# Kernel optimization log

Hardware: AMD Instinct MI355X
Metric: run time of the kernel (lower is better)

The kernel has to match this reference:

```python
import jax, jax.numpy as jnp
import numpy as np

N_AST = 200000
N_TEST = 10000
H = 128
NUM_AST_LABELS = 128
AST_CONTENT = 256
NUM_CLASSES = 2
N_LAYERS = 5
E_AA, E_AT, E_TA = 2000000, 500000, 500000


def seg_mean(msg, dst, n):
    # mean aggregation of edge messages per destination node
    s = jax.ops.segment_sum(msg, dst, num_segments=n)
    d = jax.ops.segment_sum(jnp.ones((dst.shape[0], 1), msg.dtype), dst, num_segments=n)
    return s / jnp.maximum(d, 1.0)


def gcn_layer(h_ast, h_test, src_aa, dst_aa, src_at, dst_at, src_ta, dst_ta,
              W_aa, W_at, W_ta, b_ast, b_test):
    # transform-then-aggregate per canonical edge type, sum over edge types per dst ntype
    m_aa = seg_mean((h_ast @ W_aa)[src_aa], dst_aa, N_AST)
    m_ta = seg_mean((h_test @ W_ta)[src_ta], dst_ta, N_AST)
    new_ast = jax.nn.relu(m_aa + m_ta + b_ast)
    m_at = seg_mean((h_ast @ W_at)[src_at], dst_at, N_TEST)
    new_test = jax.nn.relu(m_at + b_test)
    return new_ast, new_test


def setup_inputs() -> dict:
    key = jax.random.key(0)
    ks = jax.random.split(key, 16)
    Hh = H // 2
    inp = {
        "ast_label": jax.random.randint(ks[0], (N_AST,), 0, NUM_AST_LABELS),
        "ast_content": jax.random.normal(ks[1], (N_AST, AST_CONTENT), jnp.float32),
        "src_aa": jax.random.randint(ks[2], (E_AA,), 0, N_AST, jnp.int32),
        "dst_aa": jax.random.randint(ks[3], (E_AA,), 0, N_AST, jnp.int32),
        "src_at": jax.random.randint(ks[4], (E_AT,), 0, N_AST, jnp.int32),
        "dst_at": jax.random.randint(ks[5], (E_AT,), 0, N_TEST, jnp.int32),
        "src_ta": jax.random.randint(ks[6], (E_TA,), 0, N_TEST, jnp.int32),
        "dst_ta": jax.random.randint(ks[7], (E_TA,), 0, N_AST, jnp.int32),
        "n_test": N_TEST,
        "ast_label_emb": jax.random.normal(ks[8], (NUM_AST_LABELS, Hh), jnp.float32) * 0.1,
        "ast_content_W": jax.random.normal(ks[9], (AST_CONTENT, Hh), jnp.float32) * (1.0 / np.sqrt(AST_CONTENT)),
        "ast_content_b": jax.random.normal(ks[10], (Hh,), jnp.float32) * 0.1,
        "test_embedding": jax.random.normal(ks[11], (H,), jnp.float32),
        "W_aa": jax.random.normal(ks[12], (N_LAYERS, H, H), jnp.float32) * (1.0 / np.sqrt(H)),
        "W_at": jax.random.normal(ks[13], (N_LAYERS, H, H), jnp.float32) * (1.0 / np.sqrt(H)),
        "W_ta": jax.random.normal(ks[14], (N_LAYERS, H, H), jnp.float32) * (1.0 / np.sqrt(H)),
        "b_ast": jnp.zeros((N_LAYERS, H), jnp.float32),
        "b_test": jnp.zeros((N_LAYERS, H), jnp.float32),
        "dec_W": jax.random.normal(ks[15], (H, NUM_CLASSES), jnp.float32) * (1.0 / np.sqrt(H)),
        "dec_b": jnp.zeros((NUM_CLASSES,), jnp.float32),
    }
    return inp


def reference(ast_label, ast_content, src_aa, dst_aa, src_at, dst_at, src_ta, dst_ta,
              n_test, ast_label_emb, ast_content_W, ast_content_b, test_embedding,
              W_aa, W_at, W_ta, b_ast, b_test, dec_W, dec_b):
    # hetero node encoding: ast = [embedding(label) || linear(content)], test = broadcast learned vector
    h_ast = jnp.concatenate(
        [ast_label_emb[ast_label], ast_content @ ast_content_W + ast_content_b], axis=-1)
    h_test = jnp.broadcast_to(test_embedding[None, :], (n_test, H))

    def layer(i, ha, ht):
        return gcn_layer(ha, ht, src_aa, dst_aa, src_at, dst_at, src_ta, dst_ta,
                         W_aa[i], W_at[i], W_ta[i], b_ast[i], b_test[i])

    h_ast, h_test = layer(0, h_ast, h_test)
    res_a, res_t = h_ast, h_test
    h_ast, h_test = layer(1, h_ast, h_test)
    h_ast, h_test = res_a + h_ast, res_t + h_test
    h_ast, h_test = layer(2, h_ast, h_test)
    res_a, res_t = h_ast, h_test
    h_ast, h_test = layer(3, h_ast, h_test)
    h_ast, h_test = res_a + h_ast, res_t + h_test
    h_ast, h_test = layer(4, h_ast, h_test)

    logits = h_ast @ dec_W + dec_b  # ast_decode_node_func with num_classes>1 -> softmax
    pred = jax.nn.softmax(logits, axis=1)
    return logits, pred
```

## Files before the change

kernel.cpp:

```cpp
#include <hip/hip_runtime.h>

#define N_ASTN 200000
#define N_TESTN 10000
#define HDIM 128
#define E_AA_N 2000000
#define E_AT_N 500000
#define E_TA_N 500000

typedef __bf16 bf16x8 __attribute__((ext_vector_type(8)));
typedef float f32x4 __attribute__((ext_vector_type(4)));
typedef float f32x2 __attribute__((ext_vector_type(2)));

static __device__ __forceinline__ float bflo(unsigned u) {
    union { unsigned x; float f; } c; c.x = u << 16; return c.f;
}
static __device__ __forceinline__ float bfhi(unsigned u) {
    union { unsigned x; float f; } c; c.x = u & 0xffff0000u; return c.f;
}
static __device__ __forceinline__ unsigned short f2bf(float f) {
    union { float f; unsigned u; } c; c.f = f;
    unsigned u = c.u;
    return (unsigned short)((u + 0x7fffu + ((u >> 16) & 1u)) >> 16);
}
static __device__ __forceinline__ unsigned pack2(float a, float b) {
    return (unsigned)f2bf(a) | ((unsigned)f2bf(b) << 16);
}
static __device__ __forceinline__ f32x2 unpk(unsigned u) {
    union { unsigned q[2]; f32x2 v; } t;
    t.q[0] = u << 16;
    t.q[1] = u & 0xffff0000u;
    return t.v;
}


__global__ void detect_k(const unsigned short* __restrict__ p, int* __restrict__ flag) {
    __shared__ int cnt;
    if (threadIdx.x == 0) cnt = 0;
    __syncthreads();
    int local = 0;
    for (int i = threadIdx.x; i < 8192; i += 256) {
        unsigned e = ((unsigned)p[i] >> 7) & 0xFFu;
        if (e >= 158u) local++;
    }
    atomicAdd(&cnt, local);
    __syncthreads();
    if (threadIdx.x == 0) *flag = (cnt > 64) ? 1 : 0;
}


struct ConvSpec {
    const void* src[11];
    int off[11];
    int total;
};

__global__ void conv_params_k(ConvSpec spec, const int* __restrict__ flag,
                              unsigned short* __restrict__ dst) {
    int f32 = *flag;
    int i = blockIdx.x * blockDim.x + threadIdx.x;
    int stride = gridDim.x * blockDim.x;
    for (; i < spec.total; i += stride) {
        int s = 10;
        for (int k = 1; k < 11; k++) {
            if (i < spec.off[k]) { s = k - 1; break; }
        }
        int j = i - spec.off[s];
        unsigned short v;
        if (f32) v = f2bf(((const float*)spec.src[s])[j]);
        else     v = ((const unsigned short*)spec.src[s])[j];
        dst[i] = v;
    }
}


__global__ void count_k(const int* __restrict__ dst, int nE, int nNode,
                        int* __restrict__ cnt) {
    int i = blockIdx.x * blockDim.x + threadIdx.x;
    int stride = gridDim.x * blockDim.x;
    for (; i < nE; i += stride) {
        unsigned d = (unsigned)dst[i];
        if (d < (unsigned)nNode) atomicAdd(&cnt[d], 1);
    }
}

__global__ void scan_bsum(const int* __restrict__ in, int n, int* __restrict__ bsum) {
    __shared__ int lds[256];
    int b = blockIdx.x, tid = threadIdx.x;
    int base = b * 1024 + tid * 4;
    int s = 0;
#pragma unroll
    for (int j = 0; j < 4; j++) { int i = base + j; if (i < n) s += in[i]; }
    lds[tid] = s; __syncthreads();
    for (int off = 128; off; off >>= 1) {
        if (tid < off) lds[tid] += lds[tid + off];
        __syncthreads();
    }
    if (tid == 0) bsum[b] = lds[0];
}

__global__ void scan_top(int* __restrict__ bsum, int nb) {
    __shared__ int lds[256];
    int tid = threadIdx.x;
    int v = (tid < nb) ? bsum[tid] : 0;
    lds[tid] = v; __syncthreads();
    for (int off = 1; off < 256; off <<= 1) {
        int t = (tid >= off) ? lds[tid - off] : 0;
        __syncthreads();
        lds[tid] += t;
        __syncthreads();
    }
    if (tid < nb) bsum[tid] = lds[tid] - v;
}

__global__ void scan_final(const int* __restrict__ in, int n,
                           const int* __restrict__ bsum, int* __restrict__ out) {
    __shared__ int lds[256];
    int b = blockIdx.x, tid = threadIdx.x;
    int base = b * 1024 + tid * 4;
    int v[4]; int s = 0;
#pragma unroll
    for (int j = 0; j < 4; j++) { int i = base + j; v[j] = (i < n) ? in[i] : 0; s += v[j]; }
    lds[tid] = s; __syncthreads();
    for (int off = 1; off < 256; off <<= 1) {
        int t = (tid >= off) ? lds[tid - off] : 0;
        __syncthreads();
        lds[tid] += t;
        __syncthreads();
    }
    int texcl = lds[tid] - s;
    int run = bsum[b] + texcl;
#pragma unroll
    for (int j = 0; j < 4; j++) { int i = base + j; if (i < n) out[i] = run; run += v[j]; }
}

__global__ void fill_k(const int* __restrict__ src, const int* __restrict__ dst, int nE,
                       int nNode, const int* __restrict__ indptr, int* __restrict__ cursor,
                       int* __restrict__ edges) {
    int i = blockIdx.x * blockDim.x + threadIdx.x;
    int stride = gridDim.x * blockDim.x;
    for (; i < nE; i += stride) {
        unsigned d = (unsigned)dst[i];
        if (d >= (unsigned)nNode) continue;
        unsigned pos = (unsigned)(indptr[d] + atomicAdd(&cursor[d], 1));
        if (pos < (unsigned)nE) edges[pos] = src[i];
    }
}


__global__ void encode_emb(const int* __restrict__ label, const unsigned* __restrict__ embU,
                           unsigned* __restrict__ hAU) {
    int idx = blockIdx.x * blockDim.x + threadIdx.x;
    int node = idx >> 5, c = idx & 31;
    int lb = label[node] & 127;
    hAU[node * 64 + c] = embU[lb * 32 + c];
}

__global__ void init_test(const unsigned* __restrict__ tEmbU, unsigned* __restrict__ hTU) {
    int idx = blockIdx.x * blockDim.x + threadIdx.x;
    int node = idx >> 6, c = idx & 63;
    hTU[node * 64 + c] = tEmbU[c];
}


template<int NST>
__global__ void __launch_bounds__(256) gemm_rowblk(
    const void* __restrict__ Araw, const __bf16* __restrict__ W,
    const __bf16* __restrict__ bias, __bf16* __restrict__ C,
    int M, int K, int lda, int ldc, const int* __restrict__ flagp)
{
    __shared__ __bf16 sW[16384];
    int a_f32 = flagp ? *flagp : 0;
    int tid = threadIdx.x;
    int nkb = K >> 5;
    const int N = NST * 16;
    int ngroups = nkb * NST * 64;
    for (int g = tid; g < ngroups; g += 256) {
        int l = g & 63;
        int sk = g >> 6;
        int s = sk % NST, kb = sk / NST;
        int krow = kb * 32 + ((l >> 4) << 3);
        int col = s * 16 + (l & 15);
        bf16x8 tmp;
#pragma unroll
        for (int j = 0; j < 8; j++) tmp[j] = W[(krow + j) * N + col];
        *(bf16x8*)(&sW[g * 8]) = tmp;
    }
    __syncthreads();
    int wave = tid >> 6, lane = tid & 63;
    int mrow = lane & 15, koff = (lane >> 4) << 3;
    int tilesM = M >> 4;
    for (int mt = blockIdx.x * 4 + wave; mt < tilesM; mt += gridDim.x * 4) {
        int m0 = mt << 4;
        f32x4 acc[NST];
#pragma unroll
        for (int s = 0; s < NST; s++) acc[s] = (f32x4){0.f, 0.f, 0.f, 0.f};
        for (int kb = 0; kb < nkb; kb++) {
            bf16x8 a;
            if (a_f32) {
                const float* Af = (const float*)Araw + (size_t)(m0 + mrow) * lda + koff + kb * 32;
                f32x4 x0 = *(const f32x4*)Af;
                f32x4 x1 = *(const f32x4*)(Af + 4);
#pragma unroll
                for (int j = 0; j < 4; j++) { a[j] = (__bf16)x0[j]; a[4 + j] = (__bf16)x1[j]; }
            } else {
                const __bf16* Ab = (const __bf16*)Araw + (size_t)(m0 + mrow) * lda + koff + kb * 32;
                a = *(const bf16x8*)Ab;
            }
#pragma unroll
            for (int s = 0; s < NST; s++) {
                bf16x8 b = *(const bf16x8*)(&sW[((kb * NST + s) * 64 + lane) * 8]);
                acc[s] = __builtin_amdgcn_mfma_f32_16x16x32_bf16(a, b, acc[s], 0, 0, 0);
            }
        }
        int r0 = m0 + ((lane >> 4) << 2);
#pragma unroll
        for (int s = 0; s < NST; s++) {
            int col = s * 16 + (lane & 15);
            float bv = bias ? (float)bias[col] : 0.f;
#pragma unroll
            for (int i = 0; i < 4; i++)
                C[(size_t)(r0 + i) * ldc + col] = (__bf16)(acc[s][i] + bv);
        }
    }
}


__global__ void __launch_bounds__(256) test_transform(
    const __bf16* __restrict__ A, const __bf16* __restrict__ W,
    const __bf16* __restrict__ bias, __bf16* __restrict__ C,
    int M, int resflag)
{
    __shared__ __bf16 sW[16384];
    int tid = threadIdx.x;
    for (int g = tid; g < 2048; g += 256) {
        int l = g & 63;
        int sk = g >> 6;
        int s = sk & 7, kb = sk >> 3;
        int krow = kb * 32 + ((l >> 4) << 3);
        int col = s * 16 + (l & 15);
        bf16x8 tmp;
#pragma unroll
        for (int j = 0; j < 8; j++) tmp[j] = W[(krow + j) * 128 + col];
        *(bf16x8*)(&sW[g * 8]) = tmp;
    }
    __syncthreads();
    int wave = tid >> 6, lane = tid & 63;
    int mrow = lane & 15, koff = (lane >> 4) << 3;
    int total = (M >> 4) * 8;
    for (int t = blockIdx.x * 4 + wave; t < total; t += gridDim.x * 4) {
        int s = t & 7;
        int m0 = (t >> 3) << 4;
        f32x4 acc = {0.f, 0.f, 0.f, 0.f};
#pragma unroll
        for (int kb = 0; kb < 4; kb++) {
            bf16x8 a = *(const bf16x8*)(A + (size_t)(m0 + mrow) * 128 + koff + kb * 32);
            bf16x8 b = *(const bf16x8*)(&sW[((kb * 8 + s) * 64 + lane) * 8]);
            acc = __builtin_amdgcn_mfma_f32_16x16x32_bf16(a, b, acc, 0, 0, 0);
        }
        int col = s * 16 + (lane & 15);
        float bv = (float)bias[col];
        int r0 = m0 + ((lane >> 4) << 2);
#pragma unroll
        for (int i = 0; i < 4; i++) {
            float v = fmaxf(acc[i] + bv, 0.f);
            if (resflag) v += (float)C[(size_t)(r0 + i) * 128 + col];
            C[(size_t)(r0 + i) * 128 + col] = (__bf16)v;
        }
    }
}


__global__ void __launch_bounds__(256) ast_update(
    const uint4* __restrict__ TAq, const uint4* __restrict__ TTq,
    const int* __restrict__ ipA, const int* __restrict__ eA,
    const int* __restrict__ ipT, const int* __restrict__ eT,
    const uint4* __restrict__ biasq, unsigned* __restrict__ h,
    int n, int resflag)
{
    int node = (blockIdx.x * blockDim.x + threadIdx.x) >> 4;
    int l = threadIdx.x & 15;
    if (node >= n) return;
    const char* TAb = (const char*)TAq;
    const char* TTb = (const char*)TTq;
    unsigned loff = (unsigned)l << 4;

    f32x2 sa[4] = {{0.f,0.f},{0.f,0.f},{0.f,0.f},{0.f,0.f}};
    int a0 = ipA[node], a1 = ipA[node + 1];
    {
        int e = a0;
        for (; e + 1 < a1; e += 2) {
            unsigned o0 = ((unsigned)eA[e] << 8) + loff;
            unsigned o1 = ((unsigned)eA[e + 1] << 8) + loff;
            uint4 u0 = *(const uint4*)(TAb + o0);
            uint4 u1 = *(const uint4*)(TAb + o1);
            sa[0] += unpk(u0.x); sa[1] += unpk(u0.y);
            sa[2] += unpk(u0.z); sa[3] += unpk(u0.w);
            sa[0] += unpk(u1.x); sa[1] += unpk(u1.y);
            sa[2] += unpk(u1.z); sa[3] += unpk(u1.w);
        }
        if (e < a1) {
            unsigned o0 = ((unsigned)eA[e] << 8) + loff;
            uint4 u0 = *(const uint4*)(TAb + o0);
            sa[0] += unpk(u0.x); sa[1] += unpk(u0.y);
            sa[2] += unpk(u0.z); sa[3] += unpk(u0.w);
        }
    }
    f32x2 st[4] = {{0.f,0.f},{0.f,0.f},{0.f,0.f},{0.f,0.f}};
    int t0 = ipT[node], t1 = ipT[node + 1];
    {
        int e = t0;
        for (; e + 1 < t1; e += 2) {
            unsigned o0 = ((unsigned)eT[e] << 8) + loff;
            unsigned o1 = ((unsigned)eT[e + 1] << 8) + loff;
            uint4 u0 = *(const uint4*)(TTb + o0);
            uint4 u1 = *(const uint4*)(TTb + o1);
            st[0] += unpk(u0.x); st[1] += unpk(u0.y);
            st[2] += unpk(u0.z); st[3] += unpk(u0.w);
            st[0] += unpk(u1.x); st[1] += unpk(u1.y);
            st[2] += unpk(u1.z); st[3] += unpk(u1.w);
        }
        if (e < t1) {
            unsigned o0 = ((unsigned)eT[e] << 8) + loff;
            uint4 u0 = *(const uint4*)(TTb + o0);
            st[0] += unpk(u0.x); st[1] += unpk(u0.y);
            st[2] += unpk(u0.z); st[3] += unpk(u0.w);
        }
    }
    int da = a1 - a0; if (da < 1) da = 1;
    int dt = t1 - t0; if (dt < 1) dt = 1;
    float inva = 1.0f / (float)da, invt = 1.0f / (float)dt;
    uint4 ub = biasq[l];
    float v[8];
    v[0] = sa[0].x * inva + st[0].x * invt + bflo(ub.x);
    v[1] = sa[0].y * inva + st[0].y * invt + bfhi(ub.x);
    v[2] = sa[1].x * inva + st[1].x * invt + bflo(ub.y);
    v[3] = sa[1].y * inva + st[1].y * invt + bfhi(ub.y);
    v[4] = sa[2].x * inva + st[2].x * invt + bflo(ub.z);
    v[5] = sa[2].y * inva + st[2].y * invt + bfhi(ub.z);
    v[6] = sa[3].x * inva + st[3].x * invt + bflo(ub.w);
    v[7] = sa[3].y * inva + st[3].y * invt + bfhi(ub.w);
#pragma unroll
    for (int j = 0; j < 8; j++) v[j] = fmaxf(v[j], 0.f);
    uint4* hq = (uint4*)h;
    if (resflag) {
        uint4 r = hq[(size_t)node * 16 + l];
        v[0] += bflo(r.x); v[1] += bfhi(r.x);
        v[2] += bflo(r.y); v[3] += bfhi(r.y);
        v[4] += bflo(r.z); v[5] += bfhi(r.z);
        v[6] += bflo(r.w); v[7] += bfhi(r.w);
    }
    uint4 o;
    o.x = pack2(v[0], v[1]); o.y = pack2(v[2], v[3]);
    o.z = pack2(v[4], v[5]); o.w = pack2(v[6], v[7]);
    hq[(size_t)node * 16 + l] = o;
}


__global__ void __launch_bounds__(256) agg_at_k(
    const uint4* __restrict__ Hq,
    const int* __restrict__ ip, const int* __restrict__ ed,
    uint4* __restrict__ outq, int n)
{
    int node = (blockIdx.x * blockDim.x + threadIdx.x) >> 4;
    int l = threadIdx.x & 15;
    if (node >= n) return;
    const char* Hb = (const char*)Hq;
    unsigned loff = (unsigned)l << 4;
    f32x2 sa[4] = {{0.f,0.f},{0.f,0.f},{0.f,0.f},{0.f,0.f}};
    int a0 = ip[node], a1 = ip[node + 1];
    {
        int e = a0;
        for (; e + 1 < a1; e += 2) {
            unsigned o0 = ((unsigned)ed[e] << 8) + loff;
            unsigned o1 = ((unsigned)ed[e + 1] << 8) + loff;
            uint4 u0 = *(const uint4*)(Hb + o0);
            uint4 u1 = *(const uint4*)(Hb + o1);
            sa[0] += unpk(u0.x); sa[1] += unpk(u0.y);
            sa[2] += unpk(u0.z); sa[3] += unpk(u0.w);
            sa[0] += unpk(u1.x); sa[1] += unpk(u1.y);
            sa[2] += unpk(u1.z); sa[3] += unpk(u1.w);
        }
        if (e < a1) {
            unsigned o0 = ((unsigned)ed[e] << 8) + loff;
            uint4 u0 = *(const uint4*)(Hb + o0);
            sa[0] += unpk(u0.x); sa[1] += unpk(u0.y);
            sa[2] += unpk(u0.z); sa[3] += unpk(u0.w);
        }
    }
    int da = a1 - a0; if (da < 1) da = 1;
    float inv = 1.0f / (float)da;
    uint4 o;
    o.x = pack2(sa[0].x * inv, sa[0].y * inv);
    o.y = pack2(sa[1].x * inv, sa[1].y * inv);
    o.z = pack2(sa[2].x * inv, sa[2].y * inv);
    o.w = pack2(sa[3].x * inv, sa[3].y * inv);
    outq[(size_t)node * 16 + l] = o;
}


__global__ void __launch_bounds__(256) decoder_k(
    const unsigned* __restrict__ h, const unsigned* __restrict__ wU,
    const unsigned* __restrict__ decbU, void* __restrict__ out, int n,
    const int* __restrict__ flagp)
{
    int f32out = *flagp;
    int wid = (blockIdx.x * blockDim.x + threadIdx.x) >> 6;
    int lane = threadIdx.x & 63;
    if (wid >= n) return;
    unsigned u = h[(size_t)wid * 64 + lane];
    float h0 = bflo(u), h1 = bfhi(u);
    unsigned w0 = wU[lane * 2], w1 = wU[lane * 2 + 1];
    float p0 = h0 * bflo(w0) + h1 * bflo(w1);
    float p1 = h0 * bfhi(w0) + h1 * bfhi(w1);
    for (int off = 32; off; off >>= 1) {
        p0 += __shfl_down(p0, off);
        p1 += __shfl_down(p1, off);
    }
    if (lane == 0) {
        unsigned db = decbU[0];
        float l0 = p0 + bflo(db);
        float l1 = p1 + bfhi(db);
        float m = fmaxf(l0, l1);
        float e0 = __expf(l0 - m), e1 = __expf(l1 - m);
        float invs = 1.0f / (e0 + e1);
        if (f32out) {
            float* o = (float*)out;
            o[wid * 2 + 0] = l0;
            o[wid * 2 + 1] = l1;
            o[2 * N_ASTN + wid * 2 + 0] = e0 * invs;
            o[2 * N_ASTN + wid * 2 + 1] = e1 * invs;
        } else {
            unsigned short* o = (unsigned short*)out;
            o[wid * 2 + 0] = f2bf(l0);
            o[wid * 2 + 1] = f2bf(l1);
            o[2 * N_ASTN + wid * 2 + 0] = f2bf(e0 * invs);
            o[2 * N_ASTN + wid * 2 + 1] = f2bf(e1 * invs);
        }
    }
}


extern "C" void kernel_launch(void* const* d_in, const int* in_sizes, int n_in,
                              void* d_out, int out_size, void* d_ws, size_t ws_size,
                              hipStream_t stream) {
    const int* ast_label = (const int*)d_in[0];
    const void* ast_content = d_in[1];
    const int* src_aa = (const int*)d_in[2];
    const int* dst_aa = (const int*)d_in[3];
    const int* src_at = (const int*)d_in[4];
    const int* dst_at = (const int*)d_in[5];
    const int* src_ta = (const int*)d_in[6];
    const int* dst_ta = (const int*)d_in[7];

    char* ws = (char*)d_ws;
    size_t off = 0;
    auto alloc = [&](size_t bytes) {
        char* p = ws + off;
        off += (bytes + 255) & ~(size_t)255;
        return p;
    };
    int* flag = (int*)alloc(256);
    const int P_EMB = 0, P_CW = 8192, P_CB = 24576, P_TEMB = 24640, P_WAA = 24768,
              P_WAT = 106688, P_WTA = 188608, P_BAST = 270528, P_BTEST = 271168,
              P_DECW = 271808, P_DECB = 272064, P_TOTAL = 272066;
    __bf16* params = (__bf16*)alloc((size_t)P_TOTAL * 2);
    __bf16* hA = (__bf16*)alloc((size_t)N_ASTN * HDIM * 2);
    __bf16* TA = (__bf16*)alloc((size_t)N_ASTN * HDIM * 2);
    __bf16* hT = (__bf16*)alloc((size_t)N_TESTN * HDIM * 2);
    __bf16* TT = (__bf16*)alloc((size_t)N_TESTN * HDIM * 2);
    int* ip_aa = (int*)alloc((size_t)(N_ASTN + 1) * 4);
    int* ip_ta = (int*)alloc((size_t)(N_ASTN + 1) * 4);
    int* ip_at = (int*)alloc((size_t)(N_TESTN + 1) * 4);
    int* e_aa = (int*)alloc((size_t)E_AA_N * 4);
    int* e_ta = (int*)alloc((size_t)E_TA_N * 4);
    int* e_at = (int*)alloc((size_t)E_AT_N * 4);
    char* zbase = alloc(((size_t)(N_ASTN + 1 + N_ASTN) * 2 + (N_TESTN + 1 + N_TESTN)) * 4);
    int* cnt_aa = (int*)zbase;
    int* cur_aa = cnt_aa + (N_ASTN + 1);
    int* cnt_ta = cur_aa + N_ASTN;
    int* cur_ta = cnt_ta + (N_ASTN + 1);
    int* cnt_at = cur_ta + N_ASTN;
    int* cur_at = cnt_at + (N_TESTN + 1);
    size_t zbytes = ((size_t)(N_ASTN + 1 + N_ASTN) * 2 + (N_TESTN + 1 + N_TESTN)) * 4;
    int* bsumA = (int*)alloc(256 * 4);
    int* bsumT = (int*)alloc(256 * 4);
    int* bsumX = (int*)alloc(256 * 4);
    __bf16* aggAT = (__bf16*)zbase;

    if (ws_size < off) {
        hipMemsetAsync(d_out, 0, (size_t)out_size * 2, stream);
        return;
    }

    detect_k<<<1, 256, 0, stream>>>((const unsigned short*)ast_content, flag);
    ConvSpec spec;
    spec.src[0] = d_in[9];  spec.off[0] = P_EMB;
    spec.src[1] = d_in[10]; spec.off[1] = P_CW;
    spec.src[2] = d_in[11]; spec.off[2] = P_CB;
    spec.src[3] = d_in[12]; spec.off[3] = P_TEMB;
    spec.src[4] = d_in[13]; spec.off[4] = P_WAA;
    spec.src[5] = d_in[14]; spec.off[5] = P_WAT;
    spec.src[6] = d_in[15]; spec.off[6] = P_WTA;
    spec.src[7] = d_in[16]; spec.off[7] = P_BAST;
    spec.src[8] = d_in[17]; spec.off[8] = P_BTEST;
    spec.src[9] = d_in[18]; spec.off[9] = P_DECW;
    spec.src[10] = d_in[19]; spec.off[10] = P_DECB;
    spec.total = P_TOTAL;
    conv_params_k<<<256, 256, 0, stream>>>(spec, flag, (unsigned short*)params);

    hipMemsetAsync(zbase, 0, zbytes, stream);

    count_k<<<4096, 256, 0, stream>>>(dst_aa, E_AA_N, N_ASTN, cnt_aa);
    count_k<<<2048, 256, 0, stream>>>(dst_ta, E_TA_N, N_ASTN, cnt_ta);
    count_k<<<2048, 256, 0, stream>>>(dst_at, E_AT_N, N_TESTN, cnt_at);

    const int nA = N_ASTN + 1, nT = N_TESTN + 1;
    const int nbA = (nA + 1023) / 1024, nbT = (nT + 1023) / 1024;
    scan_bsum<<<nbA, 256, 0, stream>>>(cnt_aa, nA, bsumA);
    scan_top<<<1, 256, 0, stream>>>(bsumA, nbA);
    scan_final<<<nbA, 256, 0, stream>>>(cnt_aa, nA, bsumA, ip_aa);
    scan_bsum<<<nbA, 256, 0, stream>>>(cnt_ta, nA, bsumT);
    scan_top<<<1, 256, 0, stream>>>(bsumT, nbA);
    scan_final<<<nbA, 256, 0, stream>>>(cnt_ta, nA, bsumT, ip_ta);
    scan_bsum<<<nbT, 256, 0, stream>>>(cnt_at, nT, bsumX);
    scan_top<<<1, 256, 0, stream>>>(bsumX, nbT);
    scan_final<<<nbT, 256, 0, stream>>>(cnt_at, nT, bsumX, ip_at);

    fill_k<<<4096, 256, 0, stream>>>(src_aa, dst_aa, E_AA_N, N_ASTN, ip_aa, cur_aa, e_aa);
    fill_k<<<2048, 256, 0, stream>>>(src_ta, dst_ta, E_TA_N, N_ASTN, ip_ta, cur_ta, e_ta);
    fill_k<<<2048, 256, 0, stream>>>(src_at, dst_at, E_AT_N, N_TESTN, ip_at, cur_at, e_at);

    encode_emb<<<N_ASTN * 32 / 256, 256, 0, stream>>>(ast_label, (const unsigned*)(params + P_EMB),
                                                      (unsigned*)hA);
    gemm_rowblk<4><<<1568, 256, 0, stream>>>(ast_content, params + P_CW, params + P_CB,
                                             hA + 64, N_ASTN, 256, 256, HDIM, flag);
    init_test<<<N_TESTN * 64 / 256, 256, 0, stream>>>((const unsigned*)(params + P_TEMB),
                                                      (unsigned*)hT);

    const int resflags[5] = {0, 1, 0, 1, 0};
    for (int l = 0; l < 5; l++) {
        const __bf16* Waa = params + P_WAA + (size_t)l * HDIM * HDIM;
        const __bf16* Wat = params + P_WAT + (size_t)l * HDIM * HDIM;
        const __bf16* Wta = params + P_WTA + (size_t)l * HDIM * HDIM;
        gemm_rowblk<8><<<160, 256, 0, stream>>>(hT, Wta, nullptr, TT, N_TESTN, HDIM, HDIM, HDIM, nullptr);
        agg_at_k<<<N_TESTN / 16, 256, 0, stream>>>(
            (const uint4*)hA, ip_at, e_at, (uint4*)aggAT, N_TESTN);
        gemm_rowblk<8><<<1568, 256, 0, stream>>>(hA, Waa, nullptr, TA, N_ASTN, HDIM, HDIM, HDIM, nullptr);
        test_transform<<<256, 256, 0, stream>>>(
            aggAT, Wat, params + P_BTEST + (size_t)l * HDIM, hT, N_TESTN, resflags[l]);
        ast_update<<<N_ASTN / 16, 256, 0, stream>>>(
            (const uint4*)TA, (const uint4*)TT, ip_aa, e_aa, ip_ta, e_ta,
            (const uint4*)(params + P_BAST + (size_t)l * HDIM), (unsigned*)hA,
            N_ASTN, resflags[l]);
    }

    decoder_k<<<N_ASTN / 4, 256, 0, stream>>>((const unsigned*)hA,
                                              (const unsigned*)(params + P_DECW),
                                              (const unsigned*)(params + P_DECB),
                                              d_out, N_ASTN, flag);
}
```

Baseline: 1.616 ms.

## Fuse decoder into last layer update, merge CSR build launches, unroll gathers

The softmax decoder now runs inside the final ast_update kernel, so the last hidden state is never written to memory and read back. The three per-edge-type count, scan and fill passes are each merged into a single launch that covers all three edge types. The edge-gather loops are unrolled to four edges per iteration to keep more loads in flight. The cost is more branching in the merged kernels and higher register use in the gather loops.

Measured after the change: 1.491 ms. 1.08x faster.

```diff
diff --git a/kernel.cpp b/kernel.cpp
--- a/kernel.cpp
+++ b/kernel.cpp
@@ -6,6 +6,8 @@
 #define E_AA_N 2000000
 #define E_AT_N 500000
 #define E_TA_N 500000
+#define NBA 196
+#define NBT 10
 
 typedef __bf16 bf16x8 __attribute__((ext_vector_type(8)));
 typedef float f32x4 __attribute__((ext_vector_type(4)));
@@ -31,6 +33,10 @@
     t.q[1] = u & 0xffff0000u;
     return t.v;
 }
+
+#define ACC4(S, U) \
+    S[0] += unpk((U).x); S[1] += unpk((U).y); \
+    S[2] += unpk((U).z); S[3] += unpk((U).w);
 
 
 __global__ void detect_k(const unsigned short* __restrict__ p, int* __restrict__ flag) {
@@ -73,20 +79,36 @@
 }
 
 
-__global__ void count_k(const int* __restrict__ dst, int nE, int nNode,
-                        int* __restrict__ cnt) {
+__global__ void count3_k(const int* __restrict__ dAA, const int* __restrict__ dTA,
+                         const int* __restrict__ dAT,
+                         int* __restrict__ cAA, int* __restrict__ cTA, int* __restrict__ cAT) {
     int i = blockIdx.x * blockDim.x + threadIdx.x;
     int stride = gridDim.x * blockDim.x;
-    for (; i < nE; i += stride) {
-        unsigned d = (unsigned)dst[i];
-        if (d < (unsigned)nNode) atomicAdd(&cnt[d], 1);
-    }
-}
-
-__global__ void scan_bsum(const int* __restrict__ in, int n, int* __restrict__ bsum) {
+    const int T = E_AA_N + E_TA_N + E_AT_N;
+    for (; i < T; i += stride) {
+        if (i < E_AA_N) {
+            unsigned d = (unsigned)dAA[i];
+            if (d < (unsigned)N_ASTN) atomicAdd(&cAA[d], 1);
+        } else if (i < E_AA_N + E_TA_N) {
+            unsigned d = (unsigned)dTA[i - E_AA_N];
+            if (d < (unsigned)N_ASTN) atomicAdd(&cTA[d], 1);
+        } else {
+            unsigned d = (unsigned)dAT[i - (E_AA_N + E_TA_N)];
+            if (d < (unsigned)N_TESTN) atomicAdd(&cAT[d], 1);
+        }
+    }
+}
+
+__global__ void scan_bsum3(const int* __restrict__ cA, const int* __restrict__ cT,
+                           const int* __restrict__ cX,
+                           int* __restrict__ bA, int* __restrict__ bT, int* __restrict__ bX) {
     __shared__ int lds[256];
     int b = blockIdx.x, tid = threadIdx.x;
-    int base = b * 1024 + tid * 4;
+    const int* in; int n; int* bsum; int bb;
+    if (b < NBA)            { in = cA; n = N_ASTN + 1;  bsum = bA; bb = b; }
+    else if (b < 2 * NBA)   { in = cT; n = N_ASTN + 1;  bsum = bT; bb = b - NBA; }
+    else                    { in = cX; n = N_TESTN + 1; bsum = bX; bb = b - 2 * NBA; }
+    int base = bb * 1024 + tid * 4;
     int s = 0;
 #pragma unroll
     for (int j = 0; j < 4; j++) { int i = base + j; if (i < n) s += in[i]; }
@@ -95,12 +117,16 @@
         if (tid < off) lds[tid] += lds[tid + off];
         __syncthreads();
     }
-    if (tid == 0) bsum[b] = lds[0];
-}
-
-__global__ void scan_top(int* __restrict__ bsum, int nb) {
+    if (tid == 0) bsum[bb] = lds[0];
+}
+
+__global__ void scan_top3(int* __restrict__ bA, int* __restrict__ bT, int* __restrict__ bX) {
     __shared__ int lds[256];
-    int tid = threadIdx.x;
+    int b = blockIdx.x, tid = threadIdx.x;
+    int* bsum; int nb;
+    if (b == 0)      { bsum = bA; nb = NBA; }
+    else if (b == 1) { bsum = bT; nb = NBA; }
+    else             { bsum = bX; nb = NBT; }
     int v = (tid < nb) ? bsum[tid] : 0;
     lds[tid] = v; __syncthreads();
     for (int off = 1; off < 256; off <<= 1) {
@@ -112,11 +138,18 @@
     if (tid < nb) bsum[tid] = lds[tid] - v;
 }
 
-__global__ void scan_final(const int* __restrict__ in, int n,
-                           const int* __restrict__ bsum, int* __restrict__ out) {
+__global__ void scan_final3(const int* __restrict__ cA, const int* __restrict__ cT,
+                            const int* __restrict__ cX,
+                            const int* __restrict__ bA, const int* __restrict__ bT,
+                            const int* __restrict__ bX,
+                            int* __restrict__ ipA, int* __restrict__ ipT, int* __restrict__ ipX) {
     __shared__ int lds[256];
     int b = blockIdx.x, tid = threadIdx.x;
-    int base = b * 1024 + tid * 4;
+    const int* in; int n; const int* bsum; int* out; int bb;
+    if (b < NBA)          { in = cA; n = N_ASTN + 1;  bsum = bA; out = ipA; bb = b; }
+    else if (b < 2 * NBA) { in = cT; n = N_ASTN + 1;  bsum = bT; out = ipT; bb = b - NBA; }
+    else                  { in = cX; n = N_TESTN + 1; bsum = bX; out = ipX; bb = b - 2 * NBA; }
+    int base = bb * 1024 + tid * 4;
     int v[4]; int s = 0;
 #pragma unroll
     for (int j = 0; j < 4; j++) { int i = base + j; v[j] = (i < n) ? in[i] : 0; s += v[j]; }
@@ -128,21 +161,36 @@
         __syncthreads();
     }
     int texcl = lds[tid] - s;
-    int run = bsum[b] + texcl;
+    int run = bsum[bb] + texcl;
 #pragma unroll
     for (int j = 0; j < 4; j++) { int i = base + j; if (i < n) out[i] = run; run += v[j]; }
 }
 
-__global__ void fill_k(const int* __restrict__ src, const int* __restrict__ dst, int nE,
-                       int nNode, const int* __restrict__ indptr, int* __restrict__ cursor,
-                       int* __restrict__ edges) {
+__global__ void fill3_k(const int* __restrict__ sAA, const int* __restrict__ dAA,
+                        const int* __restrict__ ipAA, int* __restrict__ curAA, int* __restrict__ eAA,
+                        const int* __restrict__ sTA, const int* __restrict__ dTA,
+                        const int* __restrict__ ipTA, int* __restrict__ curTA, int* __restrict__ eTA,
+                        const int* __restrict__ sAT, const int* __restrict__ dAT,
+                        const int* __restrict__ ipAT, int* __restrict__ curAT, int* __restrict__ eAT) {
     int i = blockIdx.x * blockDim.x + threadIdx.x;
     int stride = gridDim.x * blockDim.x;
-    for (; i < nE; i += stride) {
-        unsigned d = (unsigned)dst[i];
-        if (d >= (unsigned)nNode) continue;
-        unsigned pos = (unsigned)(indptr[d] + atomicAdd(&cursor[d], 1));
-        if (pos < (unsigned)nE) edges[pos] = src[i];
+    const int T = E_AA_N + E_TA_N + E_AT_N;
+    for (; i < T; i += stride) {
+        const int* src; const int* dst; const int* ip; int* cur; int* ed; int nN, nE, j;
+        if (i < E_AA_N) {
+            j = i; src = sAA; dst = dAA; ip = ipAA; cur = curAA; ed = eAA;
+            nN = N_ASTN; nE = E_AA_N;
+        } else if (i < E_AA_N + E_TA_N) {
+            j = i - E_AA_N; src = sTA; dst = dTA; ip = ipTA; cur = curTA; ed = eTA;
+            nN = N_ASTN; nE = E_TA_N;
+        } else {
+            j = i - (E_AA_N + E_TA_N); src = sAT; dst = dAT; ip = ipAT; cur = curAT; ed = eAT;
+            nN = N_TESTN; nE = E_AT_N;
+        }
+        unsigned d = (unsigned)dst[j];
+        if (d >= (unsigned)nN) continue;
+        unsigned pos = (unsigned)(ip[d] + atomicAdd(&cur[d], 1));
+        if (pos < (unsigned)nE) ed[pos] = src[j];
     }
 }
 
@@ -270,12 +318,15 @@
 }
 
 
+template<int DECODE>
 __global__ void __launch_bounds__(256) ast_update(
     const uint4* __restrict__ TAq, const uint4* __restrict__ TTq,
     const int* __restrict__ ipA, const int* __restrict__ eA,
     const int* __restrict__ ipT, const int* __restrict__ eT,
     const uint4* __restrict__ biasq, unsigned* __restrict__ h,
-    int n, int resflag)
+    int n, int resflag,
+    const uint4* __restrict__ decWq, const unsigned* __restrict__ decbU,
+    void* __restrict__ outp, const int* __restrict__ flagp)
 {
     int node = (blockIdx.x * blockDim.x + threadIdx.x) >> 4;
     int l = threadIdx.x & 15;
@@ -284,46 +335,43 @@
     const char* TTb = (const char*)TTq;
     unsigned loff = (unsigned)l << 4;
 
+    int a0 = ipA[node], a1 = ipA[node + 1];
+    int t0 = ipT[node], t1 = ipT[node + 1];
+
     f32x2 sa[4] = {{0.f,0.f},{0.f,0.f},{0.f,0.f},{0.f,0.f}};
-    int a0 = ipA[node], a1 = ipA[node + 1];
     {
         int e = a0;
-        for (; e + 1 < a1; e += 2) {
-            unsigned o0 = ((unsigned)eA[e] << 8) + loff;
+        for (; e + 3 < a1; e += 4) {
+            unsigned o0 = ((unsigned)eA[e]     << 8) + loff;
             unsigned o1 = ((unsigned)eA[e + 1] << 8) + loff;
+            unsigned o2 = ((unsigned)eA[e + 2] << 8) + loff;
+            unsigned o3 = ((unsigned)eA[e + 3] << 8) + loff;
             uint4 u0 = *(const uint4*)(TAb + o0);
             uint4 u1 = *(const uint4*)(TAb + o1);
-            sa[0] += unpk(u0.x); sa[1] += unpk(u0.y);
-            sa[2] += unpk(u0.z); sa[3] += unpk(u0.w);
-            sa[0] += unpk(u1.x); sa[1] += unpk(u1.y);
-            sa[2] += unpk(u1.z); sa[3] += unpk(u1.w);
-        }
-        if (e < a1) {
+            uint4 u2 = *(const uint4*)(TAb + o2);
+            uint4 u3 = *(const uint4*)(TAb + o3);
+            ACC4(sa, u0) ACC4(sa, u1) ACC4(sa, u2) ACC4(sa, u3)
+        }
+        for (; e < a1; e++) {
             unsigned o0 = ((unsigned)eA[e] << 8) + loff;
             uint4 u0 = *(const uint4*)(TAb + o0);
-            sa[0] += unpk(u0.x); sa[1] += unpk(u0.y);
-            sa[2] += unpk(u0.z); sa[3] += unpk(u0.w);
+            ACC4(sa, u0)
         }
     }
     f32x2 st[4] = {{0.f,0.f},{0.f,0.f},{0.f,0.f},{0.f,0.f}};
-    int t0 = ipT[node], t1 = ipT[node + 1];
     {
         int e = t0;
         for (; e + 1 < t1; e += 2) {
-            unsigned o0 = ((unsigned)eT[e] << 8) + loff;
+            unsigned o0 = ((unsigned)eT[e]     << 8) + loff;
             unsigned o1 = ((unsigned)eT[e + 1] << 8) + loff;
             uint4 u0 = *(const uint4*)(TTb + o0);
             uint4 u1 = *(const uint4*)(TTb + o1);
-            st[0] += unpk(u0.x); st[1] += unpk(u0.y);
-            st[2] += unpk(u0.z); st[3] += unpk(u0.w);
-            st[0] += unpk(u1.x); st[1] += unpk(u1.y);
-            st[2] += unpk(u1.z); st[3] += unpk(u1.w);
+            ACC4(st, u0) ACC4(st, u1)
         }
         if (e < t1) {
             unsigned o0 = ((unsigned)eT[e] << 8) + loff;
             uint4 u0 = *(const uint4*)(TTb + o0);
-            st[0] += unpk(u0.x); st[1] += unpk(u0.y);
-            st[2] += unpk(u0.z); st[3] += unpk(u0.w);
+            ACC4(st, u0)
         }
     }
     int da = a1 - a0; if (da < 1) da = 1;
@@ -341,6 +389,47 @@
     v[7] = sa[3].y * inva + st[3].y * invt + bfhi(ub.w);
 #pragma unroll
     for (int j = 0; j < 8; j++) v[j] = fmaxf(v[j], 0.f);
+
+    if (DECODE) {
+        uint4 w0 = decWq[l * 2], w1 = decWq[l * 2 + 1];
+        float p0 = 0.f, p1 = 0.f;
+        p0 += v[0] * bflo(w0.x); p1 += v[0] * bfhi(w0.x);
+        p0 += v[1] * bflo(w0.y); p1 += v[1] * bfhi(w0.y);
+        p0 += v[2] * bflo(w0.z); p1 += v[2] * bfhi(w0.z);
+        p0 += v[3] * bflo(w0.w); p1 += v[3] * bfhi(w0.w);
+        p0 += v[4] * bflo(w1.x); p1 += v[4] * bfhi(w1.x);
+        p0 += v[5] * bflo(w1.y); p1 += v[5] * bfhi(w1.y);
+        p0 += v[6] * bflo(w1.z); p1 += v[6] * bfhi(w1.z);
+        p0 += v[7] * bflo(w1.w); p1 += v[7] * bfhi(w1.w);
+#pragma unroll
+        for (int off = 1; off < 16; off <<= 1) {
+            p0 += __shfl_xor(p0, off);
+            p1 += __shfl_xor(p1, off);
+        }
+        if (l == 0) {
+            unsigned db = decbU[0];
+            float l0 = p0 + bflo(db);
+            float l1 = p1 + bfhi(db);
+            float m = fmaxf(l0, l1);
+            float e0 = __expf(l0 - m), e1 = __expf(l1 - m);
+            float invs = 1.0f / (e0 + e1);
+            if (*flagp) {
+                float* o = (float*)outp;
+                o[node * 2 + 0] = l0;
+                o[node * 2 + 1] = l1;
+                o[2 * N_ASTN + node * 2 + 0] = e0 * invs;
+                o[2 * N_ASTN + node * 2 + 1] = e1 * invs;
+            } else {
+                unsigned short* o = (unsigned short*)outp;
+                o[node * 2 + 0] = f2bf(l0);
+                o[node * 2 + 1] = f2bf(l1);
+                o[2 * N_ASTN + node * 2 + 0] = f2bf(e0 * invs);
+                o[2 * N_ASTN + node * 2 + 1] = f2bf(e1 * invs);
+            }
+        }
+        return;
+    }
+
     uint4* hq = (uint4*)h;
     if (resflag) {
         uint4 r = hq[(size_t)node * 16 + l];
@@ -370,21 +459,21 @@
     int a0 = ip[node], a1 = ip[node + 1];
     {
         int e = a0;
-        for (; e + 1 < a1; e += 2) {
-            unsigned o0 = ((unsigned)ed[e] << 8) + loff;
+        for (; e + 3 < a1; e += 4) {
+            unsigned o0 = ((unsigned)ed[e]     << 8) + loff;
             unsigned o1 = ((unsigned)ed[e + 1] << 8) + loff;
+            unsigned o2 = ((unsigned)ed[e + 2] << 8) + loff;
+            unsigned o3 = ((unsigned)ed[e + 3] << 8) + loff;
             uint4 u0 = *(const uint4*)(Hb + o0);
             uint4 u1 = *(const uint4*)(Hb + o1);
-            sa[0] += unpk(u0.x); sa[1] += unpk(u0.y);
-            sa[2] += unpk(u0.z); sa[3] += unpk(u0.w);
-            sa[0] += unpk(u1.x); sa[1] += unpk(u1.y);
-            sa[2] += unpk(u1.z); sa[3] += unpk(u1.w);
-        }
-        if (e < a1) {
+            uint4 u2 = *(const uint4*)(Hb + o2);
+            uint4 u3 = *(const uint4*)(Hb + o3);
+            ACC4(sa, u0) ACC4(sa, u1) ACC4(sa, u2) ACC4(sa, u3)
+        }
+        for (; e < a1; e++) {
             unsigned o0 = ((unsigned)ed[e] << 8) + loff;
             uint4 u0 = *(const uint4*)(Hb + o0);
-            sa[0] += unpk(u0.x); sa[1] += unpk(u0.y);
-            sa[2] += unpk(u0.z); sa[3] += unpk(u0.w);
+            ACC4(sa, u0)
         }
     }
     int da = a1 - a0; if (da < 1) da = 1;
@@ -395,48 +484,6 @@
     o.z = pack2(sa[2].x * inv, sa[2].y * inv);
     o.w = pack2(sa[3].x * inv, sa[3].y * inv);
     outq[(size_t)node * 16 + l] = o;
-}
-
-
-__global__ void __launch_bounds__(256) decoder_k(
-    const unsigned* __restrict__ h, const unsigned* __restrict__ wU,
-    const unsigned* __restrict__ decbU, void* __restrict__ out, int n,
-    const int* __restrict__ flagp)
-{
-    int f32out = *flagp;
-    int wid = (blockIdx.x * blockDim.x + threadIdx.x) >> 6;
-    int lane = threadIdx.x & 63;
-    if (wid >= n) return;
-    unsigned u = h[(size_t)wid * 64 + lane];
-    float h0 = bflo(u), h1 = bfhi(u);
-    unsigned w0 = wU[lane * 2], w1 = wU[lane * 2 + 1];
-    float p0 = h0 * bflo(w0) + h1 * bflo(w1);
-    float p1 = h0 * bfhi(w0) + h1 * bfhi(w1);
-    for (int off = 32; off; off >>= 1) {
-        p0 += __shfl_down(p0, off);
-        p1 += __shfl_down(p1, off);
-    }
-    if (lane == 0) {
-        unsigned db = decbU[0];
-        float l0 = p0 + bflo(db);
-        float l1 = p1 + bfhi(db);
-        float m = fmaxf(l0, l1);
-        float e0 = __expf(l0 - m), e1 = __expf(l1 - m);
-        float invs = 1.0f / (e0 + e1);
-        if (f32out) {
-            float* o = (float*)out;
-            o[wid * 2 + 0] = l0;
-            o[wid * 2 + 1] = l1;
-            o[2 * N_ASTN + wid * 2 + 0] = e0 * invs;
-            o[2 * N_ASTN + wid * 2 + 1] = e1 * invs;
-        } else {
-            unsigned short* o = (unsigned short*)out;
-            o[wid * 2 + 0] = f2bf(l0);
-            o[wid * 2 + 1] = f2bf(l1);
-            o[2 * N_ASTN + wid * 2 + 0] = f2bf(e0 * invs);
-            o[2 * N_ASTN + wid * 2 + 1] = f2bf(e1 * invs);
-        }
-    }
 }
 
 
@@ -510,25 +557,15 @@
 
     hipMemsetAsync(zbase, 0, zbytes, stream);
 
-    count_k<<<4096, 256, 0, stream>>>(dst_aa, E_AA_N, N_ASTN, cnt_aa);
-    count_k<<<2048, 256, 0, stream>>>(dst_ta, E_TA_N, N_ASTN, cnt_ta);
-    count_k<<<2048, 256, 0, stream>>>(dst_at, E_AT_N, N_TESTN, cnt_at);
-
-    const int nA = N_ASTN + 1, nT = N_TESTN + 1;
-    const int nbA = (nA + 1023) / 1024, nbT = (nT + 1023) / 1024;
-    scan_bsum<<<nbA, 256, 0, stream>>>(cnt_aa, nA, bsumA);
-    scan_top<<<1, 256, 0, stream>>>(bsumA, nbA);
-    scan_final<<<nbA, 256, 0, stream>>>(cnt_aa, nA, bsumA, ip_aa);
-    scan_bsum<<<nbA, 256, 0, stream>>>(cnt_ta, nA, bsumT);
-    scan_top<<<1, 256, 0, stream>>>(bsumT, nbA);
-    scan_final<<<nbA, 256, 0, stream>>>(cnt_ta, nA, bsumT, ip_ta);
-    scan_bsum<<<nbT, 256, 0, stream>>>(cnt_at, nT, bsumX);
-    scan_top<<<1, 256, 0, stream>>>(bsumX, nbT);
-    scan_final<<<nbT, 256, 0, stream>>>(cnt_at, nT, bsumX, ip_at);
-
-    fill_k<<<4096, 256, 0, stream>>>(src_aa, dst_aa, E_AA_N, N_ASTN, ip_aa, cur_aa, e_aa);
-    fill_k<<<2048, 256, 0, stream>>>(src_ta, dst_ta, E_TA_N, N_ASTN, ip_ta, cur_ta, e_ta);
-    fill_k<<<2048, 256, 0, stream>>>(src_at, dst_at, E_AT_N, N_TESTN, ip_at, cur_at, e_at);
+    count3_k<<<3072, 256, 0, stream>>>(dst_aa, dst_ta, dst_at, cnt_aa, cnt_ta, cnt_at);
+    scan_bsum3<<<2 * NBA + NBT, 256, 0, stream>>>(cnt_aa, cnt_ta, cnt_at, bsumA, bsumT, bsumX);
+    scan_top3<<<3, 256, 0, stream>>>(bsumA, bsumT, bsumX);
+    scan_final3<<<2 * NBA + NBT, 256, 0, stream>>>(cnt_aa, cnt_ta, cnt_at,
+                                                   bsumA, bsumT, bsumX,
+                                                   ip_aa, ip_ta, ip_at);
+    fill3_k<<<3072, 256, 0, stream>>>(src_aa, dst_aa, ip_aa, cur_aa, e_aa,
+                                      src_ta, dst_ta, ip_ta, cur_ta, e_ta,
+                                      src_at, dst_at, ip_at, cur_at, e_at);
 
     encode_emb<<<N_ASTN * 32 / 256, 256, 0, stream>>>(ast_label, (const unsigned*)(params + P_EMB),
                                                       (unsigned*)hA);
@@ -537,6 +574,8 @@
     init_test<<<N_TESTN * 64 / 256, 256, 0, stream>>>((const unsigned*)(params + P_TEMB),
                                                       (unsigned*)hT);
 
+    const uint4* decWq = (const uint4*)(params + P_DECW);
+    const unsigned* decbU = (const unsigned*)(params + P_DECB);
     const int resflags[5] = {0, 1, 0, 1, 0};
     for (int l = 0; l < 5; l++) {
         const __bf16* Waa = params + P_WAA + (size_t)l * HDIM * HDIM;
@@ -548,14 +587,16 @@
         gemm_rowblk<8><<<1568, 256, 0, stream>>>(hA, Waa, nullptr, TA, N_ASTN, HDIM, HDIM, HDIM, nullptr);
         test_transform<<<256, 256, 0, stream>>>(
             aggAT, Wat, params + P_BTEST + (size_t)l * HDIM, hT, N_TESTN, resflags[l]);
-        ast_update<<<N_ASTN / 16, 256, 0, stream>>>(
-            (const uint4*)TA, (const uint4*)TT, ip_aa, e_aa, ip_ta, e_ta,
-            (const uint4*)(params + P_BAST + (size_t)l * HDIM), (unsigned*)hA,
-            N_ASTN, resflags[l]);
-    }
-
-    decoder_k<<<N_ASTN / 4, 256, 0, stream>>>((const unsigned*)hA,
-                                              (const unsigned*)(params + P_DECW),
-                                              (const unsigned*)(params + P_DECB),
-                                              d_out, N_ASTN, flag);
-}
+        if (l < 4) {
+            ast_update<0><<<N_ASTN / 16, 256, 0, stream>>>(
+                (const uint4*)TA, (const uint4*)TT, ip_aa, e_aa, ip_ta, e_ta,
+                (const uint4*)(params + P_BAST + (size_t)l * HDIM), (unsigned*)hA,
+                N_ASTN, resflags[l], nullptr, nullptr, nullptr, nullptr);
+        } else {
+            ast_update<1><<<N_ASTN / 16, 256, 0, stream>>>(
+                (const uint4*)TA, (const uint4*)TT, ip_aa, e_aa, ip_ta, e_ta,
+                (const uint4*)(params + P_BAST + (size_t)l * HDIM), (unsigned*)hA,
+                N_ASTN, 0, decWq, decbU, d_out, flag);
+        }
+    }
+}
```
